# Performance work log

Hardware: AMD Instinct MI355X
Metric: run time of the kernel (lower is better)

Reference implementation:

```python
import jax, jax.numpy as jnp
import numpy as np

N = 30000
E = 480000
D_IN = 128
EPS = 1e-5
NEG_SLOPE = 0.2
# (in_dim, out_channels, heads) per GATConv layer; concat=True everywhere (PyG default)
CFG = [(D_IN, 100, 5), (500, 50, 5), (250, 32, 4), (128, 8, 4), (32, 1, 1)]
BN_DIMS = (500, 250, 128)


def setup_inputs() -> dict:
    key = jax.random.key(0)
    ks = iter(jax.random.split(key, 80))
    inp = {
        "x": jax.random.normal(next(ks), (N, D_IN), jnp.float32),
        "edge_index": jax.random.randint(next(ks), (2, E), 0, N),
        "edge_weight": jax.random.uniform(next(ks), (E, 1), jnp.float32),
    }
    for l, (cin, cout, h) in enumerate(CFG, 1):
        s = 1.0 / np.sqrt(cin)
        inp[f"W{l}"] = jax.random.normal(next(ks), (cin, h * cout), jnp.float32) * s
        inp[f"a_s{l}"] = jax.random.normal(next(ks), (1, h, cout), jnp.float32) * 0.1
        inp[f"a_d{l}"] = jax.random.normal(next(ks), (1, h, cout), jnp.float32) * 0.1
        inp[f"We{l}"] = jax.random.normal(next(ks), (1, h * cout), jnp.float32)
        inp[f"a_e{l}"] = jax.random.normal(next(ks), (1, h, cout), jnp.float32) * 0.1
        inp[f"b{l}"] = jnp.zeros((h * cout,), jnp.float32)
    for l, d in zip((1, 2, 3), BN_DIMS):
        inp[f"g{l}"] = jnp.ones((d,), jnp.float32)
        inp[f"beta{l}"] = jnp.zeros((d,), jnp.float32)
    return inp


def _gat(x, src, dst, ea, W, a_s, a_d, We, a_e, b, heads, cout):
    """PyG GATConv with edge_dim attention (concat=True)."""
    n = x.shape[0]
    h = (x @ W).reshape(n, heads, cout)            # [N,H,C]
    e = (ea @ We).reshape(-1, heads, cout)         # [E,H,C]
    al_src = (h * a_s).sum(-1)                     # [N,H]
    al_dst = (h * a_d).sum(-1)                     # [N,H]
    logit = jax.nn.leaky_relu(al_src[src] + al_dst[dst] + (e * a_e).sum(-1), NEG_SLOPE)
    m = jax.ops.segment_max(logit, dst, num_segments=n)
    m = jnp.where(jnp.isfinite(m), m, 0.0)
    ex = jnp.exp(logit - m[dst])                   # [E,H]
    den = jax.ops.segment_sum(ex, dst, num_segments=n)
    alpha = ex / jnp.maximum(den[dst], 1e-16)      # segment softmax over in-edges of dst
    out = jax.ops.segment_sum(h[src] * alpha[..., None], dst, num_segments=n)
    return out.reshape(n, heads * cout) + b


def _bn(x, g, b):
    mu = x.mean(0)
    var = x.var(0)  # biased, as torch uses for normalization
    return (x - mu) * jax.lax.rsqrt(var + EPS) * g + b


def reference(x, edge_index, edge_weight,
              W1, a_s1, a_d1, We1, a_e1, b1,
              W2, a_s2, a_d2, We2, a_e2, b2,
              W3, a_s3, a_d3, We3, a_e3, b3,
              W4, a_s4, a_d4, We4, a_e4, b4,
              W5, a_s5, a_d5, We5, a_e5, b5,
              g1, beta1, g2, beta2, g3, beta3):
    # add self loops (PyG default) with edge_attr fill_value='mean'
    loop = jnp.arange(N)
    src = jnp.concatenate([edge_index[0], loop])
    dst = jnp.concatenate([edge_index[1], loop])
    ea = jnp.concatenate([edge_weight, jnp.full((N, 1), edge_weight.mean(), edge_weight.dtype)], axis=0)

    h = _gat(x, src, dst, ea, W1, a_s1, a_d1, We1, a_e1, b1, 5, 100)
    h = jax.nn.relu(_bn(h, g1, beta1))
    h = _gat(h, src, dst, ea, W2, a_s2, a_d2, We2, a_e2, b2, 5, 50)
    h = jax.nn.relu(_bn(h, g2, beta2))
    h = _gat(h, src, dst, ea, W3, a_s3, a_d3, We3, a_e3, b3, 4, 32)
    h = jax.nn.relu(_bn(h, g3, beta3))
    h = _gat(h, src, dst, ea, W4, a_s4, a_d4, We4, a_e4, b4, 4, 8)
    h = jax.nn.relu(h)
    h = _gat(h, src, dst, ea, W5, a_s5, a_d5, We5, a_e5, b5, 1, 1)
    return h
```

## Files before the change

### kernel.cpp

```cpp
#include <hip/hip_runtime.h>
#include <hip/hip_bf16.h>
#include <math.h>

#define NN 30000
#define EE 480000
#define ET (EE + NN)
#define NEG_SLOPE 0.2f
#define BN_EPS 1e-5f

struct LayerCfg { int cin, C, H; };
static const LayerCfg g_cfg[5] = {
    {128, 100, 5}, {500, 50, 5}, {250, 32, 4}, {128, 8, 4}, {32, 1, 1}
};

typedef short short8 __attribute__((ext_vector_type(8)));
typedef unsigned short u16x8 __attribute__((ext_vector_type(8)));
typedef float f32x4 __attribute__((ext_vector_type(4)));

__device__ __forceinline__ unsigned short f2bf(float f) {
    unsigned int u = __builtin_bit_cast(unsigned int, f);
    u = (u + 0x7FFFu + ((u >> 16) & 1u)) >> 16;
    return (unsigned short)u;
}
__device__ __forceinline__ float bf2f(unsigned short h) {
    unsigned int u = ((unsigned int)h) << 16;
    return __builtin_bit_cast(float, u);
}


struct PrepArgs {
    const float* W[5];
    const float* We[5];
    const float* ae[5];
    unsigned short* bh[5];
    unsigned short* bl[5];
    float* wedot;
    int K[5], N[5], Kp[5], Np[5], C[5], H[5];
};

static const int EBLK = (ET + 255) / 256;

__global__ void prep_fused_kernel(const int* __restrict__ ei, int* __restrict__ rank,
                                  int* __restrict__ cnt, const float* __restrict__ ew,
                                  float* __restrict__ esum, PrepArgs a) {
    __shared__ float sdata[256];
    __shared__ float tile[32][33];
    int b = blockIdx.x;
    int tid = threadIdx.x;

    if (b < EBLK) {
        int e = b * 256 + tid;
        if (e < ET) {
            int d = (e < EE) ? ei[EE + e] : (e - EE);
            rank[e] = atomicAdd(&cnt[d], 1);
        }
        return;
    }
    b -= EBLK;
    if (b < 256) {
        float s = 0.f;
        for (int i = b * 256 + tid; i < EE; i += 65536)
            s += ew[i];
        sdata[tid] = s;
        __syncthreads();
        for (int off = 128; off > 0; off >>= 1) {
            if (tid < off) sdata[tid] += sdata[tid + off];
            __syncthreads();
        }
        if (tid == 0) atomicAdd(esum, sdata[0]);
        return;
    }
    b -= 256;
    int bx = b & 15, by = (b >> 4) & 15, bz = b >> 8;
    int l = bz;
    int tx = tid & 31, ty = tid >> 5;
    if (bx == 0 && by == 0 && ty == 0 && tx < 8) {
        int hd = tx;
        if (hd < a.H[l]) {
            int C = a.C[l];
            const float* We = a.We[l] + hd * C;
            const float* ae = a.ae[l] + hd * C;
            float s = 0.f;
            for (int c = 0; c < C; c++) s += We[c] * ae[c];
            a.wedot[l * 8 + hd] = s;
        }
    }
    int Kp = a.Kp[l], Np = a.Np[l], K = a.K[l], N = a.N[l];
    int kb = bx * 32, nb = by * 32;
    if (kb >= Kp || nb >= Np) return;
    const float* B = a.W[l];
    unsigned short* Bth = a.bh[l];
    unsigned short* Btl = a.bl[l];
#pragma unroll
    for (int i = 0; i < 4; i++) {
        int k = kb + ty + i * 8, n = nb + tx;
        tile[ty + i * 8][tx] = (k < K && n < N) ? B[(size_t)k * N + n] : 0.f;
    }
    __syncthreads();
#pragma unroll
    for (int i = 0; i < 4; i++) {
        int n = nb + ty + i * 8, k = kb + tx;
        if (n < Np && k < Kp) {
            float v = tile[tx][ty + i * 8];
            unsigned short hi = f2bf(v);
            unsigned short lo = f2bf(v - bf2f(hi));
            size_t idx = (size_t)n * Kp + k;
            Bth[idx] = hi;
            Btl[idx] = lo;
        }
    }
}

__global__ void scan_kernel(const int* __restrict__ cnt, int* __restrict__ off) {
    __shared__ int lsum[1024];
    const int T = 1024;
    int t = threadIdx.x;
    int chunk = (NN + T - 1) / T;
    int base = t * chunk;
    int end = min(NN, base + chunk);
    int s = 0;
    for (int i = base; i < end; i++) s += cnt[i];
    lsum[t] = s;
    __syncthreads();
    for (int d = 1; d < T; d <<= 1) {
        int v = (t >= d) ? lsum[t - d] : 0;
        __syncthreads();
        lsum[t] += v;
        __syncthreads();
    }
    int run = (t == 0) ? 0 : lsum[t - 1];
    for (int i = base; i < end; i++) {
        off[i] = run;
        run += cnt[i];
    }
    if (t == 0) off[NN] = ET;
}

__global__ void fill_kernel(const int* __restrict__ ei, const int* __restrict__ rank,
                            const float* __restrict__ ew, const float* __restrict__ esum,
                            const int* __restrict__ off,
                            int* __restrict__ csr_src, float* __restrict__ csr_ea) {
    int e = blockIdx.x * blockDim.x + threadIdx.x;
    if (e >= ET) return;
    int sv, d;
    if (e < EE) { sv = ei[e]; d = ei[EE + e]; }
    else        { sv = e - EE; d = e - EE; }
    int p = off[d] + rank[e];
    csr_src[p] = sv;
    csr_ea[p]  = (e < EE) ? ew[e] : esum[0] * (1.0f / (float)EE);
}

#define GBM 128
#define GBNT 128
#define GBK 32
#define ASTR 36
__global__ __launch_bounds__(256) void gemm_split_kernel(const float* __restrict__ A,
                                                         const unsigned short* __restrict__ Bt_hi,
                                                         const unsigned short* __restrict__ Bt_lo,
                                                         float* __restrict__ Cm,
                                                         unsigned short* __restrict__ Ch16,
                                                         int M, int Kp, int Nc,
                                                         const float* __restrict__ colsum,
                                                         const float* __restrict__ colsumsq,
                                                         const float* __restrict__ g,
                                                         const float* __restrict__ beta,
                                                         int D) {
    __shared__ short AsH[GBM * ASTR];
    __shared__ short AsL[GBM * ASTR];
    __shared__ short BsH[GBNT * ASTR];
    __shared__ short BsL[GBNT * ASTR];
    __shared__ float sscale[512];
    __shared__ float sshift[512];
    int tid = threadIdx.x;
    bool bn = (colsum != nullptr);
    if (bn) {
        for (int c = tid; c < Kp; c += 256) {
            float sc = 0.f, sh = 0.f;
            if (c < D) {
                float mu = colsum[c] * (1.0f / (float)NN);
                float var = colsumsq[c] * (1.0f / (float)NN) - mu * mu;
                sc = g[c] * rsqrtf(var + BN_EPS);
                sh = beta[c] - mu * sc;
            }
            sscale[c] = sc;
            sshift[c] = sh;
        }
        __syncthreads();
    }
    int wave = tid >> 6, lane = tid & 63;
    int q = lane >> 4, r = lane & 15;
    int m0 = blockIdx.y * GBM, n0 = blockIdx.x * GBNT;
    int wm = (wave & 1) * 64, wn = (wave >> 1) * 64;
    f32x4 acc[4][4];
#pragma unroll
    for (int i = 0; i < 4; i++)
#pragma unroll
        for (int j = 0; j < 4; j++) acc[i][j] = (f32x4)(0.f);

    int arow2 = tid >> 1;
    int acol2 = (tid & 1) * 16;
    int brow = tid >> 2;
    int bcol = (tid & 3) * 8;

    int ksteps = Kp / GBK;
    for (int ks = 0; ks < ksteps; ks++) {
        int k0 = ks * GBK;
        {
            int m = m0 + arow2;
            float v[16];
            if (m < M) {
                const float* Ap = A + (size_t)m * Kp + k0 + acol2;
                float4 f0 = *(const float4*)(Ap);
                float4 f1 = *(const float4*)(Ap + 4);
                float4 f2 = *(const float4*)(Ap + 8);
                float4 f3 = *(const float4*)(Ap + 12);
                v[0]=f0.x; v[1]=f0.y; v[2]=f0.z; v[3]=f0.w;
                v[4]=f1.x; v[5]=f1.y; v[6]=f1.z; v[7]=f1.w;
                v[8]=f2.x; v[9]=f2.y; v[10]=f2.z; v[11]=f2.w;
                v[12]=f3.x; v[13]=f3.y; v[14]=f3.z; v[15]=f3.w;
                if (bn) {
                    int cb = k0 + acol2;
#pragma unroll
                    for (int i = 0; i < 16; i++)
                        v[i] = fmaxf(v[i] * sscale[cb + i] + sshift[cb + i], 0.f);
                }
            } else {
#pragma unroll
                for (int i = 0; i < 16; i++) v[i] = 0.f;
            }
#pragma unroll
            for (int i = 0; i < 16; i++) {
                unsigned short hi = f2bf(v[i]);
                unsigned short lo = f2bf(v[i] - bf2f(hi));
                AsH[arow2 * ASTR + acol2 + i] = (short)hi;
                AsL[arow2 * ASTR + acol2 + i] = (short)lo;
            }
        }
#pragma unroll
        for (int p = 0; p < 2; p++) {
            int row = p * 64 + brow;
            size_t gidx = (size_t)(n0 + row) * Kp + k0 + bcol;
            *((uint4*)(BsH + row * ASTR + bcol)) = *((const uint4*)(Bt_hi + gidx));
            *((uint4*)(BsL + row * ASTR + bcol)) = *((const uint4*)(Bt_lo + gidx));
        }
        __syncthreads();
        short8 ah[4], al[4], bh[4], bl[4];
#pragma unroll
        for (int i = 0; i < 4; i++) {
            ah[i] = *((const short8*)(AsH + (wm + i * 16 + r) * ASTR + q * 8));
            al[i] = *((const short8*)(AsL + (wm + i * 16 + r) * ASTR + q * 8));
        }
#pragma unroll
        for (int j = 0; j < 4; j++) {
            bh[j] = *((const short8*)(BsH + (wn + j * 16 + r) * ASTR + q * 8));
            bl[j] = *((const short8*)(BsL + (wn + j * 16 + r) * ASTR + q * 8));
        }
#pragma unroll
        for (int i = 0; i < 4; i++)
#pragma unroll
            for (int j = 0; j < 4; j++) {
                acc[i][j] = __builtin_amdgcn_mfma_f32_16x16x32_bf16(ah[i], bh[j], acc[i][j], 0, 0, 0);
                acc[i][j] = __builtin_amdgcn_mfma_f32_16x16x32_bf16(ah[i], bl[j], acc[i][j], 0, 0, 0);
                acc[i][j] = __builtin_amdgcn_mfma_f32_16x16x32_bf16(al[i], bh[j], acc[i][j], 0, 0, 0);
            }
        __syncthreads();
    }
#pragma unroll
    for (int i = 0; i < 4; i++) {
#pragma unroll
        for (int j = 0; j < 4; j++) {
#pragma unroll
            for (int reg = 0; reg < 4; reg++) {
                int mrow = m0 + wm + i * 16 + q * 4 + reg;
                int ncol = n0 + wn + j * 16 + r;
                if (mrow < M && ncol < Nc) {
                    float val = acc[i][j][reg];
                    if (Cm)   Cm[(size_t)mrow * Nc + ncol] = val;
                    if (Ch16) Ch16[(size_t)mrow * Nc + ncol] = f2bf(val);
                }
            }
        }
    }
}

__global__ void gemv_l5_kernel(const float* __restrict__ X, const float* __restrict__ W,
                               const float* __restrict__ a_s, const float* __restrict__ a_d,
                               float* __restrict__ h, float* __restrict__ al_src,
                               float* __restrict__ al_dst) {
    __shared__ float w[32];
    if (threadIdx.x < 32) w[threadIdx.x] = W[threadIdx.x];
    __syncthreads();
    int n = blockIdx.x * blockDim.x + threadIdx.x;
    if (n >= NN) return;
    const float* row = X + (size_t)n * 32;
    float s = 0.f;
#pragma unroll
    for (int i = 0; i < 8; i++) {
        float4 f = *(const float4*)(row + i * 4);
        s += f.x * w[i * 4] + f.y * w[i * 4 + 1] + f.z * w[i * 4 + 2] + f.w * w[i * 4 + 3];
    }
    h[n] = s;
    al_src[n] = s * a_s[0];
    al_dst[n] = s * a_d[0];
}

__global__ void al_wave_h16_kernel(const unsigned short* __restrict__ h16,
                                   const float* __restrict__ a_s,
                                   const float* __restrict__ a_d,
                                   float* __restrict__ al_src, float* __restrict__ al_dst,
                                   int H, int C, int HCp) {
    int w = (blockIdx.x * blockDim.x + threadIdx.x) >> 6;
    int lane = threadIdx.x & 63;
    if (w >= NN) return;
    const unsigned short* row = h16 + (size_t)w * HCp;
    float s1[5] = {0.f, 0.f, 0.f, 0.f, 0.f};
    float s2[5] = {0.f, 0.f, 0.f, 0.f, 0.f};
#pragma unroll
    for (int hd = 0; hd < 5; hd++) {
        if (hd >= H) break;
        int base = hd * C;
        for (int c = lane * 2; c < C; c += 128) {
            unsigned int u = *(const unsigned int*)(row + base + c);
            float v0 = bf2f((unsigned short)(u & 0xffffu));
            float v1 = bf2f((unsigned short)(u >> 16));
            s1[hd] += v0 * a_s[base + c] + v1 * a_s[base + c + 1];
            s2[hd] += v0 * a_d[base + c] + v1 * a_d[base + c + 1];
        }
    }
#pragma unroll
    for (int hd = 0; hd < 5; hd++) {
        if (hd >= H) break;
#pragma unroll
        for (int off = 32; off > 0; off >>= 1) {
            s1[hd] += __shfl_xor(s1[hd], off, 64);
            s2[hd] += __shfl_xor(s2[hd], off, 64);
        }
    }
    if (lane == 0) {
#pragma unroll
        for (int hd = 0; hd < 5; hd++) {
            if (hd >= H) break;
            al_src[(size_t)w * H + hd] = s1[hd];
            al_dst[(size_t)w * H + hd] = s2[hd];
        }
    }
}

__global__ void attn_kernel(const float* __restrict__ al_src,
                            const float* __restrict__ al_dst,
                            const int* __restrict__ csr_src,
                            const float* __restrict__ csr_ea,
                            const float* __restrict__ we_dot,
                            const int* __restrict__ off,
                            float* __restrict__ alpha_t, int H, int NH) {
    int t = blockIdx.x * blockDim.x + threadIdx.x;
    if (t >= NH) return;
    int n = t / H, hd = t - n * H;
    int s = off[n], e = off[n + 1];
    float ad = al_dst[(size_t)n * H + hd];
    float wd = we_dot[hd];
    float* arow = alpha_t + (size_t)hd * ET;
    float m = -INFINITY, l = 0.f;
    int p = s;
    for (; p + 3 < e; p += 4) {
        int s0 = csr_src[p], s1 = csr_src[p + 1], s2 = csr_src[p + 2], s3 = csr_src[p + 3];
        float w0 = csr_ea[p], w1 = csr_ea[p + 1], w2 = csr_ea[p + 2], w3 = csr_ea[p + 3];
        float l0 = al_src[(size_t)s0 * H + hd] + ad + w0 * wd;
        float l1 = al_src[(size_t)s1 * H + hd] + ad + w1 * wd;
        float l2 = al_src[(size_t)s2 * H + hd] + ad + w2 * wd;
        float l3 = al_src[(size_t)s3 * H + hd] + ad + w3 * wd;
        l0 = (l0 >= 0.f) ? l0 : NEG_SLOPE * l0;
        l1 = (l1 >= 0.f) ? l1 : NEG_SLOPE * l1;
        l2 = (l2 >= 0.f) ? l2 : NEG_SLOPE * l2;
        l3 = (l3 >= 0.f) ? l3 : NEG_SLOPE * l3;
        arow[p] = l0; arow[p + 1] = l1; arow[p + 2] = l2; arow[p + 3] = l3;
        float mq = fmaxf(fmaxf(l0, l1), fmaxf(l2, l3));
        float nm = fmaxf(m, mq);
        l = l * __expf(m - nm)
          + __expf(l0 - nm) + __expf(l1 - nm) + __expf(l2 - nm) + __expf(l3 - nm);
        m = nm;
    }
    for (; p < e; p++) {
        float lg = al_src[(size_t)csr_src[p] * H + hd] + ad + csr_ea[p] * wd;
        lg = (lg >= 0.f) ? lg : NEG_SLOPE * lg;
        arow[p] = lg;
        float nm = fmaxf(m, lg);
        l = l * __expf(m - nm) + __expf(lg - nm);
        m = nm;
    }
    float inv = 1.f / fmaxf(l, 1e-16f);
    for (p = s; p < e; p++) arow[p] = __expf(arow[p] - m) * inv;
}

__global__ void aggregate_v8h_kernel(const unsigned short* __restrict__ h16,
                                     const float* __restrict__ alpha_t,
                                     const int* __restrict__ off,
                                     const int* __restrict__ csr_src,
                                     const float* __restrict__ bias,
                                     float* __restrict__ out,
                                     int C, int H, int HC, int hp, int hp8,
                                     int total8, int relu, int opitch) {
    int t = blockIdx.x * blockDim.x + threadIdx.x;
    if (t >= total8) return;
    int n = t / hp8, j8 = t - n * hp8;
    int j = j8 * 8;
    int hdA = j / C;
    int hdB = (j + 7) / C;
    int bnd = (hdA + 1) * C - j;
    bnd = (bnd > 8) ? 8 : bnd;
    float mA = (hdA < H) ? 1.f : 0.f;
    float mB = (hdB < H) ? 1.f : 0.f;
    const float* arA = alpha_t + (size_t)((hdA < H) ? hdA : 0) * ET;
    const float* arB = alpha_t + (size_t)((hdB < H) ? hdB : 0) * ET;
    int s = off[n], e = off[n + 1];
    const unsigned short* hb = h16 + j;
    float acc[8];
#pragma unroll
    for (int c = 0; c < 8; c++) acc[c] = 0.f;
    int p = s;
    for (; p + 3 < e; p += 4) {
        int idx[4]; float aA[4], aB[4];
#pragma unroll
        for (int u = 0; u < 4; u++) {
            idx[u] = csr_src[p + u];
            aA[u] = arA[p + u];
            aB[u] = arB[p + u];
        }
#pragma unroll
        for (int u = 0; u < 4; u++) {
            u16x8 uv = *(const u16x8*)(hb + (size_t)idx[u] * hp);
#pragma unroll
            for (int c = 0; c < 8; c++) {
                float av = (c < bnd) ? aA[u] : aB[u];
                acc[c] += av * bf2f(uv[c]);
            }
        }
    }
    for (; p < e; p++) {
        int i0 = csr_src[p];
        float aA0 = arA[p], aB0 = arB[p];
        u16x8 uv = *(const u16x8*)(hb + (size_t)i0 * hp);
#pragma unroll
        for (int c = 0; c < 8; c++) {
            float av = (c < bnd) ? aA0 : aB0;
            acc[c] += av * bf2f(uv[c]);
        }
    }
    float o[8];
#pragma unroll
    for (int c = 0; c < 8; c++) {
        float m = (c < bnd) ? mA : mB;
        float bi = (j + c < HC) ? bias[j + c] : 0.f;
        o[c] = acc[c] * m + bi;
        if (relu) o[c] = fmaxf(o[c], 0.f);
    }
    float* op = out + (size_t)n * opitch + j;
    *(float4*)(op)     = make_float4(o[0], o[1], o[2], o[3]);
    *(float4*)(op + 4) = make_float4(o[4], o[5], o[6], o[7]);
}

__global__ void aggregate_kernel(const float* __restrict__ hfeat,
                                 const float* __restrict__ alpha_t,
                                 const int* __restrict__ off, const int* __restrict__ csr_src,
                                 const float* __restrict__ bias, float* __restrict__ out,
                                 int total) {
    int t = blockIdx.x * blockDim.x + threadIdx.x;
    if (t >= total) return;
    int n = t;
    int s = off[n], e = off[n + 1];
    float acc = 0.f;
    int p = s;
    for (; p + 3 < e; p += 4) {
        acc += alpha_t[p] * hfeat[csr_src[p]]
             + alpha_t[p + 1] * hfeat[csr_src[p + 1]]
             + alpha_t[p + 2] * hfeat[csr_src[p + 2]]
             + alpha_t[p + 3] * hfeat[csr_src[p + 3]];
    }
    for (; p < e; p++) acc += alpha_t[p] * hfeat[csr_src[p]];
    out[n] = acc + bias[0];
}


__global__ void bn_stats_kernel(const float* __restrict__ x, float* __restrict__ colsum,
                                float* __restrict__ colsumsq, int D, int pitch) {
    int rows_per_block = (NN + gridDim.x - 1) / gridDim.x;
    int r0 = blockIdx.x * rows_per_block;
    int r1 = min(NN, r0 + rows_per_block);
    int c0 = threadIdx.x;
    int c1 = threadIdx.x + 256;
    float s0 = 0.f, q0 = 0.f, s1 = 0.f, q1 = 0.f;
    for (int r = r0; r < r1; r++) {
        const float* row = x + (size_t)r * pitch;
        if (c0 < D) { float v = row[c0]; s0 += v; q0 += v * v; }
        if (c1 < D) { float v = row[c1]; s1 += v; q1 += v * v; }
    }
    if (c0 < D) { atomicAdd(&colsum[c0], s0); atomicAdd(&colsumsq[c0], q0); }
    if (c1 < D) { atomicAdd(&colsum[c1], s1); atomicAdd(&colsumsq[c1], q1); }
}


static inline size_t align_up(size_t v, size_t a) { return (v + a - 1) / a * a; }

extern "C" void kernel_launch(void* const* d_in, const int* in_sizes, int n_in,
                              void* d_out, int out_size, void* d_ws, size_t ws_size,
                              hipStream_t stream) {
    const float* x_in = (const float*)d_in[0];
    const int* ei     = (const int*)d_in[1];
    const float* ew   = (const float*)d_in[2];

    char* pws = (char*)d_ws;
    size_t off_b = 0;
    auto alloc = [&](size_t bytes) -> void* {
        void* rp = pws + off_b;
        off_b = align_up(off_b + bytes, 256);
        return rp;
    };
    float* B0      = (float*)alloc((size_t)NN * 4);
    float* B1      = (float*)alloc((size_t)NN * 512 * 4);
    unsigned short* H16 = (unsigned short*)alloc((size_t)NN * 504 * 2);
    float* alpha_t = (float*)alloc((size_t)ET * 5 * 4);
    unsigned short* Wt_hi = (unsigned short*)alloc((size_t)600 * 512 * 2);
    unsigned short* Wt_lo = (unsigned short*)alloc((size_t)600 * 512 * 2);
    float* al_src  = (float*)alloc((size_t)NN * 5 * 4);
    float* al_dst  = (float*)alloc((size_t)NN * 5 * 4);
    float* csr_ea  = (float*)alloc((size_t)ET * 4);
    int* rankb     = (int*)alloc((size_t)ET * 4);
    int* csr_src   = (int*)alloc((size_t)ET * 4);
    int* offarr    = (int*)alloc((size_t)(NN + 1) * 4);
    float* we_dot  = (float*)alloc(40 * 4);
    float* esum    = (float*)alloc(4);
    int* cnt       = (int*)alloc((size_t)NN * 4);
    float* colsum_all   = (float*)alloc(3 * 512 * 4);
    float* colsumsq_all = (float*)alloc(3 * 512 * 4);
    char* zero_end = pws + off_b;
    (void)ws_size; (void)n_in; (void)in_sizes; (void)out_size;

    int Kp[5], Np[5], hp[5];
    size_t wtoff[5];
    size_t acc_off = 0;
    for (int l = 0; l < 5; l++) {
        int K = g_cfg[l].cin, HC = g_cfg[l].C * g_cfg[l].H;
        Kp[l] = (K + 31) / 32 * 32;
        Np[l] = (HC + 127) / 128 * 128;
        hp[l] = (HC + 7) / 8 * 8;
        wtoff[l] = acc_off;
        acc_off += (size_t)Kp[l] * Np[l];
    }

    PrepArgs pa;
    for (int l = 0; l < 5; l++) {
        pa.W[l]  = (const float*)d_in[3 + l * 6 + 0];
        pa.We[l] = (const float*)d_in[3 + l * 6 + 3];
        pa.ae[l] = (const float*)d_in[3 + l * 6 + 4];
        pa.bh[l] = Wt_hi + wtoff[l];
        pa.bl[l] = Wt_lo + wtoff[l];
        pa.K[l] = g_cfg[l].cin;
        pa.N[l] = g_cfg[l].C * g_cfg[l].H;
        pa.Kp[l] = Kp[l];
        pa.Np[l] = Np[l];
        pa.C[l] = g_cfg[l].C;
        pa.H[l] = g_cfg[l].H;
    }
    pa.wedot = we_dot;

    hipMemsetAsync(esum, 0, (size_t)(zero_end - (char*)esum), stream);
    int ebl = EBLK;
    prep_fused_kernel<<<ebl + 256 + 1280, 256, 0, stream>>>(ei, rankb, cnt, ew, esum, pa);
    scan_kernel<<<1, 1024, 0, stream>>>(cnt, offarr);
    fill_kernel<<<ebl, 256, 0, stream>>>(ei, rankb, ew, esum, offarr, csr_src, csr_ea);

    for (int l = 0; l < 5; l++) {
        const LayerCfg& cf = g_cfg[l];
        int H = cf.H, C = cf.C;
        int HC = H * C;
        const float* a_s = (const float*)d_in[3 + l * 6 + 1];
        const float* a_d = (const float*)d_in[3 + l * 6 + 2];
        const float* b   = (const float*)d_in[3 + l * 6 + 5];

        const float* X = (l == 0) ? x_in : B1;
        float* outbuf = (l == 4) ? (float*)d_out : B1;
        int opitch = (l == 4) ? 1 : Kp[l + 1];
        int NH = NN * H;
        int alblocks = (NN * 64 + 255) / 256;

        if (l == 4) {
            gemv_l5_kernel<<<(NN + 255) / 256, 256, 0, stream>>>(
                X, pa.W[4], a_s, a_d, B0, al_src, al_dst);
        } else {
            const float* cs = (l >= 1) ? colsum_all + (l - 1) * 512 : nullptr;
            const float* cq = (l >= 1) ? colsumsq_all + (l - 1) * 512 : nullptr;
            const float* gg = (l >= 1) ? (const float*)d_in[33 + (l - 1) * 2 + 0] : nullptr;
            const float* bb = (l >= 1) ? (const float*)d_in[33 + (l - 1) * 2 + 1] : nullptr;
            int Din = (l >= 1) ? g_cfg[l - 1].C * g_cfg[l - 1].H : 0;
            dim3 ggrid(Np[l] / GBNT, (NN + GBM - 1) / GBM);
            gemm_split_kernel<<<ggrid, 256, 0, stream>>>(X, Wt_hi + wtoff[l], Wt_lo + wtoff[l],
                                                         nullptr, H16,
                                                         NN, Kp[l], hp[l], cs, cq, gg, bb, Din);
            al_wave_h16_kernel<<<alblocks, 256, 0, stream>>>(H16, a_s, a_d, al_src, al_dst, H, C, hp[l]);
        }

        attn_kernel<<<(NH + 255) / 256, 256, 0, stream>>>(al_src, al_dst, csr_src, csr_ea,
                                                          we_dot + l * 8, offarr, alpha_t, H, NH);

        if (l == 4) {
            aggregate_kernel<<<(NN + 255) / 256, 256, 0, stream>>>(
                B0, alpha_t, offarr, csr_src, b, outbuf, NN);
        } else {
            int hp8 = hp[l] / 8;
            int total8 = NN * hp8;
            aggregate_v8h_kernel<<<(total8 + 255) / 256, 256, 0, stream>>>(
                H16, alpha_t, offarr, csr_src, b, outbuf, C, H, HC, hp[l], hp8, total8,
                (l == 3) ? 1 : 0, opitch);
        }

        if (l < 3) {
            bn_stats_kernel<<<512, 256, 0, stream>>>(outbuf, colsum_all + l * 512,
                                                     colsumsq_all + l * 512, HC, opitch);
        }
    }
}
```

Baseline: 830.6 us.

## Restructure aggregation into column slabs interleaved across blocks for L2 locality

Replaces the per-node 8-column aggregation kernel with a slab kernel. Each thread handles 4 bf16 columns, and the block index is interleaved so that 8 consecutive blocks cover different column slabs or node ranges, which may spread gathers over the XCD L2 caches. Feature pitch is padded to a multiple of 64 for wide layers so slabs are uniform. The cost is more threads re-reading the CSR indices and alpha per node, plus extra padding in the bf16 buffer.

```diff
diff --git a/kernel.cpp b/kernel.cpp
--- a/kernel.cpp
+++ b/kernel.cpp
@@ -14,7 +14,6 @@
 };
 
 typedef short short8 __attribute__((ext_vector_type(8)));
-typedef unsigned short u16x8 __attribute__((ext_vector_type(8)));
 typedef float f32x4 __attribute__((ext_vector_type(4)));
 
 __device__ __forceinline__ unsigned short f2bf(float f) {
@@ -392,31 +391,41 @@
     for (p = s; p < e; p++) arow[p] = __expf(arow[p] - m) * inv;
 }
 
-__global__ void aggregate_v8h_kernel(const unsigned short* __restrict__ h16,
-                                     const float* __restrict__ alpha_t,
-                                     const int* __restrict__ off,
-                                     const int* __restrict__ csr_src,
-                                     const float* __restrict__ bias,
-                                     float* __restrict__ out,
-                                     int C, int H, int HC, int hp, int hp8,
-                                     int total8, int relu, int opitch) {
-    int t = blockIdx.x * blockDim.x + threadIdx.x;
-    if (t >= total8) return;
-    int n = t / hp8, j8 = t - n * hp8;
-    int j = j8 * 8;
+__global__ void aggregate_slab_kernel(const unsigned short* __restrict__ h16,
+                                      const float* __restrict__ alpha_t,
+                                      const int* __restrict__ off,
+                                      const int* __restrict__ csr_src,
+                                      const float* __restrict__ bias,
+                                      float* __restrict__ out,
+                                      int C, int H, int HC, int hp,
+                                      int lns, int lcps, int npr,
+                                      int relu, int opitch) {
+    int vs = blockIdx.x & 7;
+    int nb = blockIdx.x >> 3;
+    int slab = vs & ((1 << lns) - 1);
+    int rep  = vs >> lns;
+    int tid = threadIdx.x;
+    int cps = 1 << lcps;
+    int lc = tid & (cps - 1);
+    int ln = tid >> lcps;
+    int npb = 256 >> lcps;
+    int nl = nb * npb + ln;
+    if (nl >= npr) return;
+    int n = rep * npr + nl;
+    int j = (slab << (lcps + 2)) + (lc << 2);
+
     int hdA = j / C;
-    int hdB = (j + 7) / C;
+    int hdB = (j + 3) / C;
     int bnd = (hdA + 1) * C - j;
-    bnd = (bnd > 8) ? 8 : bnd;
+    bnd = (bnd > 4) ? 4 : bnd;
     float mA = (hdA < H) ? 1.f : 0.f;
     float mB = (hdB < H) ? 1.f : 0.f;
     const float* arA = alpha_t + (size_t)((hdA < H) ? hdA : 0) * ET;
     const float* arB = alpha_t + (size_t)((hdB < H) ? hdB : 0) * ET;
+
     int s = off[n], e = off[n + 1];
     const unsigned short* hb = h16 + j;
-    float acc[8];
-#pragma unroll
-    for (int c = 0; c < 8; c++) acc[c] = 0.f;
+    float ac0 = 0.f, ac1 = 0.f, ac2 = 0.f, ac3 = 0.f;
     int p = s;
     for (; p + 3 < e; p += 4) {
         int idx[4]; float aA[4], aB[4];
@@ -428,35 +437,31 @@
         }
 #pragma unroll
         for (int u = 0; u < 4; u++) {
-            u16x8 uv = *(const u16x8*)(hb + (size_t)idx[u] * hp);
-#pragma unroll
-            for (int c = 0; c < 8; c++) {
-                float av = (c < bnd) ? aA[u] : aB[u];
-                acc[c] += av * bf2f(uv[c]);
-            }
+            ushort4 uv = *(const ushort4*)(hb + (size_t)idx[u] * hp);
+            ac0 += ((0 < bnd) ? aA[u] : aB[u]) * bf2f(uv.x);
+            ac1 += ((1 < bnd) ? aA[u] : aB[u]) * bf2f(uv.y);
+            ac2 += ((2 < bnd) ? aA[u] : aB[u]) * bf2f(uv.z);
+            ac3 += ((3 < bnd) ? aA[u] : aB[u]) * bf2f(uv.w);
         }
     }
     for (; p < e; p++) {
         int i0 = csr_src[p];
         float aA0 = arA[p], aB0 = arB[p];
-        u16x8 uv = *(const u16x8*)(hb + (size_t)i0 * hp);
-#pragma unroll
-        for (int c = 0; c < 8; c++) {
-            float av = (c < bnd) ? aA0 : aB0;
-            acc[c] += av * bf2f(uv[c]);
-        }
-    }
-    float o[8];
-#pragma unroll
-    for (int c = 0; c < 8; c++) {
-        float m = (c < bnd) ? mA : mB;
-        float bi = (j + c < HC) ? bias[j + c] : 0.f;
-        o[c] = acc[c] * m + bi;
-        if (relu) o[c] = fmaxf(o[c], 0.f);
-    }
-    float* op = out + (size_t)n * opitch + j;
-    *(float4*)(op)     = make_float4(o[0], o[1], o[2], o[3]);
-    *(float4*)(op + 4) = make_float4(o[4], o[5], o[6], o[7]);
+        ushort4 uv = *(const ushort4*)(hb + (size_t)i0 * hp);
+        ac0 += ((0 < bnd) ? aA0 : aB0) * bf2f(uv.x);
+        ac1 += ((1 < bnd) ? aA0 : aB0) * bf2f(uv.y);
+        ac2 += ((2 < bnd) ? aA0 : aB0) * bf2f(uv.z);
+        ac3 += ((3 < bnd) ? aA0 : aB0) * bf2f(uv.w);
+    }
+    float o0 = ac0 * ((0 < bnd) ? mA : mB) + ((j + 0 < HC) ? bias[j + 0] : 0.f);
+    float o1 = ac1 * ((1 < bnd) ? mA : mB) + ((j + 1 < HC) ? bias[j + 1] : 0.f);
+    float o2 = ac2 * ((2 < bnd) ? mA : mB) + ((j + 2 < HC) ? bias[j + 2] : 0.f);
+    float o3 = ac3 * ((3 < bnd) ? mA : mB) + ((j + 3 < HC) ? bias[j + 3] : 0.f);
+    if (relu) {
+        o0 = fmaxf(o0, 0.f); o1 = fmaxf(o1, 0.f);
+        o2 = fmaxf(o2, 0.f); o3 = fmaxf(o3, 0.f);
+    }
+    *(float4*)(out + (size_t)n * opitch + j) = make_float4(o0, o1, o2, o3);
 }
 
 __global__ void aggregate_kernel(const float* __restrict__ hfeat,
@@ -517,7 +522,7 @@
     };
     float* B0      = (float*)alloc((size_t)NN * 4);
     float* B1      = (float*)alloc((size_t)NN * 512 * 4);
-    unsigned short* H16 = (unsigned short*)alloc((size_t)NN * 504 * 2);
+    unsigned short* H16 = (unsigned short*)alloc((size_t)NN * 512 * 2);
     float* alpha_t = (float*)alloc((size_t)ET * 5 * 4);
     unsigned short* Wt_hi = (unsigned short*)alloc((size_t)600 * 512 * 2);
     unsigned short* Wt_lo = (unsigned short*)alloc((size_t)600 * 512 * 2);
@@ -542,7 +547,7 @@
         int K = g_cfg[l].cin, HC = g_cfg[l].C * g_cfg[l].H;
         Kp[l] = (K + 31) / 32 * 32;
         Np[l] = (HC + 127) / 128 * 128;
-        hp[l] = (HC + 7) / 8 * 8;
+        hp[l] = (HC >= 64) ? ((HC + 63) / 64 * 64) : ((HC + 7) / 8 * 8);
         wtoff[l] = acc_off;
         acc_off += (size_t)Kp[l] * Np[l];
     }
@@ -606,11 +611,17 @@
             aggregate_kernel<<<(NN + 255) / 256, 256, 0, stream>>>(
                 B0, alpha_t, offarr, csr_src, b, outbuf, NN);
         } else {
-            int hp8 = hp[l] / 8;
-            int total8 = NN * hp8;
-            aggregate_v8h_kernel<<<(total8 + 255) / 256, 256, 0, stream>>>(
-                H16, alpha_t, offarr, csr_src, b, outbuf, C, H, HC, hp[l], hp8, total8,
-                (l == 3) ? 1 : 0, opitch);
+            int cps = (hp[l] >= 64) ? 16 : 8;
+            int lcps = (cps == 16) ? 4 : 3;
+            int nslabs = hp[l] / (cps * 4);
+            int lns = (nslabs == 8) ? 3 : (nslabs == 4) ? 2 : (nslabs == 2) ? 1 : 0;
+            int dup = 8 / nslabs;
+            int npr = NN / dup;
+            int npb = 256 / cps;
+            int gx = 8 * ((npr + npb - 1) / npb);
+            aggregate_slab_kernel<<<gx, 256, 0, stream>>>(
+                H16, alpha_t, offarr, csr_src, b, outbuf,
+                C, H, HC, hp[l], lns, lcps, npr, (l == 3) ? 1 : 0, opitch);
         }
 
         if (l < 3) {
```

Result: no change. 821.3 us (-1.1%).
